# Kernel optimization log

Hardware: AMD Instinct MI355X
Metric: run time of the kernel (lower is better)

## Reference

```python
import jax, jax.numpy as jnp
import numpy as np
from jax import lax

B, T, K, HID, NCLS = 32, 2048, 17, 64, 10
DILATIONS = (1, 1, 2)
RESIDUAL = (False, True, True)
TK = 3  # temporal kernel
BN_EPS = 1e-5
LN_EPS = 1e-5

COCO_EDGES = [(0,1),(0,2),(1,3),(2,4),(5,6),(5,7),(7,9),(6,8),(8,10),(5,11),(6,12),(11,13),(13,15),(12,14),(14,16)]

def build_skeleton_adj(num_kpts=K):
    adj = np.eye(num_kpts, dtype=np.float32)
    for i, j in COCO_EDGES:
        adj[i, j] = 1.0
        adj[j, i] = 1.0
    adj = adj + np.eye(num_kpts, dtype=np.float32)
    deg = adj.sum(axis=1, keepdims=True)
    deg[deg == 0] = 1.0
    return adj / deg

def setup_inputs() -> dict:
    key = jax.random.key(0)
    ks = jax.random.split(key, 8)
    kpts = jax.random.normal(ks[0], (B, T, K, 3), dtype=jnp.float32)
    adj = jnp.asarray(build_skeleton_adj(K))
    gcn_w0 = jax.random.normal(ks[1], (3, HID), dtype=jnp.float32) * (1.0 / np.sqrt(3))
    gcn_w1 = jax.random.normal(ks[2], (HID, HID), dtype=jnp.float32) * (1.0 / np.sqrt(HID))
    gcn_w2 = jax.random.normal(ks[3], (HID, HID), dtype=jnp.float32) * (1.0 / np.sqrt(HID))
    tcn_w = jax.random.normal(ks[4], (3, HID, HID, TK, 1), dtype=jnp.float32) * (1.0 / np.sqrt(HID * TK))
    bn_scale = 1.0 + 0.1 * jax.random.normal(ks[5], (3, HID), dtype=jnp.float32)
    bn_bias = 0.1 * jax.random.normal(ks[6], (3, HID), dtype=jnp.float32)
    bn_mean = 0.1 * jax.random.normal(ks[7], (3, HID), dtype=jnp.float32)
    bn_var = 0.5 + jax.random.uniform(jax.random.fold_in(key, 7), (3, HID), dtype=jnp.float32)
    ln_scale = jnp.ones((HID,), dtype=jnp.float32)
    ln_bias = jnp.zeros((HID,), dtype=jnp.float32)
    fc_w = jax.random.normal(jax.random.fold_in(key, 8), (HID, NCLS), dtype=jnp.float32) * (1.0 / np.sqrt(HID))
    fc_b = jnp.zeros((NCLS,), dtype=jnp.float32)
    return dict(kpts=kpts, adj=adj, gcn_w0=gcn_w0, gcn_w1=gcn_w1, gcn_w2=gcn_w2,
                tcn_w=tcn_w, bn_scale=bn_scale, bn_bias=bn_bias, bn_mean=bn_mean,
                bn_var=bn_var, ln_scale=ln_scale, ln_bias=ln_bias, fc_w=fc_w, fc_b=fc_b)

def _stgn_block(x, adj, gw, tw, bs, bb, bm, bv, dilation, residual):
    # x: [B, C_in, T, K]
    y = jnp.einsum('bctk,kv->bctv', x, adj)          # graph conv over keypoints
    y = jnp.einsum('bitk,io->botk', y, gw)           # channel mixing (intended GCN weight)
    pad = (TK - 1) * dilation // 2
    y = lax.conv_general_dilated(y, tw, window_strides=(1, 1),
                                 padding=[(pad, pad), (0, 0)],
                                 rhs_dilation=(dilation, 1),
                                 dimension_numbers=('NCHW', 'OIHW', 'NCHW'))
    inv = (bs / jnp.sqrt(bv + BN_EPS))[None, :, None, None]
    y = y * inv + (bb - bs * bm / jnp.sqrt(bv + BN_EPS))[None, :, None, None]
    y = jax.nn.relu(y)
    if residual:
        y = y + x
    return y

def reference(kpts, adj, gcn_w0, gcn_w1, gcn_w2, tcn_w, bn_scale, bn_bias, bn_mean,
              bn_var, ln_scale, ln_bias, fc_w, fc_b):
    x = jnp.transpose(kpts, (0, 3, 1, 2))  # [B, 3, T, K]
    gws = (gcn_w0, gcn_w1, gcn_w2)
    for i in range(3):
        x = _stgn_block(x, adj, gws[i], tcn_w[i], bn_scale[i], bn_bias[i],
                        bn_mean[i], bn_var[i], DILATIONS[i], RESIDUAL[i])
    feat = x.mean(axis=(2, 3))  # [B, HID] temporal/spatial mean pool
    mu = feat.mean(axis=-1, keepdims=True)
    var = feat.var(axis=-1, keepdims=True)
    feat = (feat - mu) / jnp.sqrt(var + LN_EPS) * ln_scale + ln_bias
    return feat @ fc_w + fc_b  # [B, NCLS]
```

## Files before the change

kernel.cpp:

```cpp
#include <hip/hip_runtime.h>
#include <hip/hip_fp16.h>
#include <math.h>

#define T_DIM 2048
#define TP_DIM 2052
#define K_DIM 17
#define HID   64
#define B_DIM 32

typedef short s16x8 __attribute__((ext_vector_type(8)));
typedef unsigned u32x2 __attribute__((ext_vector_type(2)));
typedef float f32x4 __attribute__((ext_vector_type(4)));
typedef _Float16 f16x2 __attribute__((ext_vector_type(2)));

__device__ __forceinline__ unsigned pkh(float lo, float hi) {
    return __builtin_bit_cast(unsigned, __builtin_amdgcn_cvt_pkrtz(lo, hi));
}
__device__ __forceinline__ f16x2 u2h(unsigned v) {
    return __builtin_bit_cast(f16x2, v);
}
__device__ __forceinline__ unsigned h2u(f16x2 v) {
    return __builtin_bit_cast(unsigned, v);
}
__device__ __forceinline__ short f2h(float f) {
    _Float16 h = (_Float16)f;
    return __builtin_bit_cast(short, h);
}

static constexpr int NBR_PTR[18] = {0,3,6,9,11,13,17,21,24,27,29,31,34,37,40,43,45,47};
static constexpr int NBR_K[47] = {
    0,1,2,  0,1,3,  0,2,4,  1,3,  2,4,
    5,6,7,11,  5,6,8,12,  5,7,9,  6,8,10,  7,9,  8,10,
    5,11,13,  6,12,14,  11,13,15,  12,14,16,  13,15,  14,16 };
__device__ const int d_NBR_PTR[18] = {0,3,6,9,11,13,17,21,24,27,29,31,34,37,40,43,45,47};
__device__ const int d_NBR_K[47] = {
    0,1,2,  0,1,3,  0,2,4,  1,3,  2,4,
    5,6,7,11,  5,6,8,12,  5,7,9,  6,8,10,  7,9,  8,10,
    5,11,13,  6,12,14,  11,13,15,  12,14,16,  13,15,  14,16 };

__global__ void fold_weights_kernel(
    const float* __restrict__ gw0, const float* __restrict__ gw1,
    const float* __restrict__ gw2, const float* __restrict__ tcn,
    const float* __restrict__ bns, const float* __restrict__ bnb,
    const float* __restrict__ bnm, const float* __restrict__ bnv,
    short* __restrict__ effT0, short* __restrict__ effT12,
    float* __restrict__ bnc)
{
    int tid = blockIdx.x * blockDim.x + threadIdx.x;
    int stride = gridDim.x * blockDim.x;
    for (int idx = tid; idx < 2048; idx += stride) {
        int o = idx >> 5, k = idx & 31, dt = k >> 3, cin = k & 7;
        float s = 0.f;
        if (dt < 3 && cin < 3)
            for (int m = 0; m < 64; m++)
                s += gw0[cin * 64 + m] * tcn[(o * 64 + m) * 3 + dt];
        effT0[idx] = f2h(s);
    }
    for (int idx = tid; idx < 24576; idx += stride) {
        int blk = idx / 12288;
        int r = idx - blk * 12288;
        int o = r / 192, k = r - o * 192, dt = k >> 6, c = k & 63;
        const float* gw = blk ? gw2 : gw1;
        const float* tw = tcn + (size_t)(blk + 1) * 64 * 64 * 3;
        float s = 0.f;
        for (int m = 0; m < 64; m++)
            s += gw[c * 64 + m] * tw[(o * 64 + m) * 3 + dt];
        effT12[idx] = f2h(s);
    }
    for (int i = tid; i < 192; i += stride) {
        float inv = bns[i] * rsqrtf(bnv[i] + 1e-5f);
        bnc[i] = inv;
        bnc[192 + i] = bnb[i] - bnm[i] * inv;
    }
}

__global__ __launch_bounds__(256) void premix_kernel(
    const float* __restrict__ x, const float* __restrict__ adj,
    float* __restrict__ xg, short* __restrict__ y2g, int cb)
{
    const int idx = blockIdx.x * 256 + threadIdx.x;
    const int total = cb * TP_DIM * K_DIM;
    if (idx < total) {
        const int b = idx / (TP_DIM * K_DIM);
        const int rem = idx - b * (TP_DIM * K_DIM);
        const int tp = rem / K_DIM, j = rem - tp * K_DIM;
        const int t = tp - 2;
        float a0 = 0.f, a1 = 0.f, a2 = 0.f;
        if (t >= 0 && t < T_DIM) {
            const float* xp = x + ((size_t)b * T_DIM + t) * 51;
            const int p0 = d_NBR_PTR[j], p1 = d_NBR_PTR[j + 1];
            for (int e = p0; e < p1; e++) {
                int k = d_NBR_K[e];
                float w = adj[k * 17 + j];
                a0 += w * xp[k * 3 + 0];
                a1 += w * xp[k * 3 + 1];
                a2 += w * xp[k * 3 + 2];
            }
        }
        float* op = xg + ((size_t)b * TP_DIM + tp) * 52 + j * 3;
        op[0] = a0; op[1] = a1; op[2] = a2;
    }
    const int zn = cb * 4 * 1088;
    for (int z = idx; z < zn; z += gridDim.x * 256) {
        int bb = z / (4 * 1088);
        int rr = z - bb * 4 * 1088;
        int pi = rr / 1088;
        int ci = rr - pi * 1088;
        int tp = (pi < 2) ? pi : (2048 + pi);
        y2g[((size_t)(bb * TP_DIM + tp) * K_DIM) * 64 + ci] = 0;
    }
}

__global__ __launch_bounds__(256, 4) void stgcn_ab_kernel(
    const float* __restrict__ xg, const float* __restrict__ adj,
    const short* __restrict__ effT0, const short* __restrict__ effT12,
    const float* __restrict__ bnc, short* __restrict__ y2g,
    float* __restrict__ part2, int b0)
{
    __shared__ unsigned adj_h[289];
    __shared__ __align__(16) float xtg[12 * 52];
    __shared__ __align__(16) short ybuf[170 * 72];

    float* pr = (float*)&ybuf[136 * 72];

    const int tid = threadIdx.x;
    const int b = blockIdx.y;
    const int t0 = blockIdx.x * 8;
    const int lane = tid & 63, wave = tid >> 6;
    const int col = lane & 15, kgrp = lane >> 4;

    for (int i = tid; i < 289; i += 256) {
        float w = adj[i];
        adj_h[i] = pkh(w, w);
    }
    {
        const float4* src = (const float4*)(xg + ((size_t)b * TP_DIM + t0) * 52);
        float4* dst = (float4*)xtg;
        for (int i = tid; i < 156; i += 256) dst[i] = src[i];
    }
    s16x8 af1 = *(const s16x8*)(effT0 + (wave * 16 + col) * 32 + kgrp * 8);
    s16x8 af2[6];
    #pragma unroll
    for (int kk = 0; kk < 6; kk++)
        af2[kk] = *(const s16x8*)(effT12 +
            (wave * 16 + col) * 192 + kk * 32 + kgrp * 8);
    __syncthreads();

    {
        f32x4 inv4 = *(const f32x4*)&bnc[wave * 16 + kgrp * 4];
        f32x4 sh4  = *(const f32x4*)&bnc[192 + wave * 16 + kgrp * 4];
        for (int tile = 0; tile < 11; tile++) {
            const int r = tile * 16 + col;
            const int me = r < 170 ? r : 169;
            const int s = (me * 241) >> 12;
            const int j = me - s * 17;
            int4 bz = {0, 0, 0, 0};
            if (kgrp < 3) {
                const float* xp = &xtg[(s + kgrp) * 52 + j * 3];
                bz.x = (int)pkh(xp[0], xp[1]);
                bz.y = (int)pkh(xp[2], 0.f);
            }
            s16x8 bfr = __builtin_bit_cast(s16x8, bz);
            f32x4 acc = __builtin_amdgcn_mfma_f32_16x16x32_f16(
                af1, bfr, (f32x4){0.f, 0.f, 0.f, 0.f}, 0, 0, 0);
            const int t = t0 - 1 + s;
            const bool valid = (t >= 0) && (t < T_DIM);
            if (r < 170) {
                float v0 = valid ? fmaxf(acc[0] * inv4[0] + sh4[0], 0.f) : 0.f;
                float v1 = valid ? fmaxf(acc[1] * inv4[1] + sh4[1], 0.f) : 0.f;
                float v2 = valid ? fmaxf(acc[2] * inv4[2] + sh4[2], 0.f) : 0.f;
                float v3 = valid ? fmaxf(acc[3] * inv4[3] + sh4[3], 0.f) : 0.f;
                u32x2 st; st[0] = pkh(v0, v1); st[1] = pkh(v2, v3);
                *(u32x2*)&ybuf[r * 72 + wave * 16 + kgrp * 4] = st;
            }
        }
    }
    __syncthreads();

    f32x4 acc2[9];
    #pragma unroll
    for (int t2 = 0; t2 < 9; t2++) acc2[t2] = (f32x4){0.f, 0.f, 0.f, 0.f};
    #pragma unroll
    for (int kk = 0; kk < 6; kk++) {
        #pragma unroll
        for (int t2 = 0; t2 < 9; t2++) {
            const int r = t2 * 16 + col;
            const int me = r < 136 ? r : 135;
            s16x8 bfr = *(const s16x8*)&ybuf[
                (me + 17 * (kk >> 1)) * 72 + (kk & 1) * 32 + kgrp * 8];
            acc2[t2] = __builtin_amdgcn_mfma_f32_16x16x32_f16(
                af2[kk], bfr, acc2[t2], 0, 0, 0);
        }
    }
    unsigned rv[17];
    {
        const int tl = tid >> 5, o0 = (tid & 31) * 2;
        #pragma unroll
        for (int v = 0; v < 17; v++)
            rv[v] = *(const unsigned*)&ybuf[((tl + 1) * 17 + v) * 72 + o0];
    }
    __syncthreads();

    #pragma unroll
    for (int t2 = 0; t2 < 9; t2++) {
        const int r = t2 * 16 + col;
        if (r < 136) {
            u32x2 st;
            st[0] = pkh(acc2[t2][0], acc2[t2][1]);
            st[1] = pkh(acc2[t2][2], acc2[t2][3]);
            *(u32x2*)&ybuf[r * 72 + wave * 16 + kgrp * 4] = st;
        }
    }
    __syncthreads();

    {
        const int tl = tid >> 5, o0 = (tid & 31) * 2;
        const f16x2 inv2 = u2h(pkh(bnc[64 + o0], bnc[64 + o0 + 1]));
        const f16x2 sh2  = u2h(pkh(bnc[256 + o0], bnc[256 + o0 + 1]));
        const f16x2 zero = u2h(0u);
        f16x2 zk[17];
        #pragma unroll
        for (int k = 0; k < 17; k++)
            zk[k] = u2h(*(const unsigned*)&ybuf[(tl * 17 + k) * 72 + o0]);
        f16x2 y2v[17];
        f16x2 pool = zero;
        #pragma unroll
        for (int v = 0; v < 17; v++) {
            f16x2 g = zero;
            #pragma unroll
            for (int e = NBR_PTR[v]; e < NBR_PTR[v + 1]; e++) {
                int k = NBR_K[e];
                g = u2h(adj_h[k * 17 + v]) * zk[k] + g;
            }
            f16x2 val = __builtin_elementwise_max(g * inv2 + sh2, zero);
            val = val + u2h(rv[v]);
            y2v[v] = val;
            pool = pool + val;
        }
        const size_t gout = ((size_t)b * TP_DIM + t0 + tl + 2) * K_DIM * 64;
        #pragma unroll
        for (int j = 0; j < 17; j++) {
            f16x2 gg = zero;
            #pragma unroll
            for (int e = NBR_PTR[j]; e < NBR_PTR[j + 1]; e++) {
                int k = NBR_K[e];
                gg = u2h(adj_h[k * 17 + j]) * y2v[k] + gg;
            }
            *(unsigned*)&y2g[gout + (size_t)j * 64 + o0] = h2u(gg);
        }
        pr[tl * 64 + o0]     = (float)pool[0];
        pr[tl * 64 + o0 + 1] = (float)pool[1];
    }
    __syncthreads();
    if (tid < 64) {
        float s = 0.f;
        #pragma unroll
        for (int i = 0; i < 8; i++) s += pr[i * 64 + tid];
        part2[((size_t)(b0 + b) * 256 + blockIdx.x) * 64 + tid] = s;
    }
}

__global__ __launch_bounds__(256, 5) void stgcn_c_kernel(
    const short* __restrict__ y2g, const short* __restrict__ effW3,
    const float* __restrict__ bnc, float* __restrict__ part, int b0)
{
    __shared__ __align__(16) short ybuf[204 * 72];
    __shared__ float pr[64];

    const int tid = threadIdx.x;
    const int b = blockIdx.y;
    const int t0 = blockIdx.x * 8;
    const int lane = tid & 63, wave = tid >> 6;
    const int col = lane & 15, kgrp = lane >> 4;

    s16x8 af3[6];
    #pragma unroll
    for (int kk = 0; kk < 6; kk++)
        af3[kk] = *(const s16x8*)(effW3 +
            (wave * 16 + col) * 192 + kk * 32 + kgrp * 8);
    const f32x4 inv4 = *(const f32x4*)&bnc[128 + wave * 16 + kgrp * 4];
    const f32x4 sh4  = *(const f32x4*)&bnc[320 + wave * 16 + kgrp * 4];

    {
        const short* base = y2g + ((size_t)b * TP_DIM + t0) * K_DIM * 64;
        for (int idx = tid; idx < 1632; idx += 256) {
            const int row = idx >> 3, c = idx & 7;
            *(s16x8*)&ybuf[row * 72 + c * 8] =
                *(const s16x8*)(base + (size_t)row * 64 + c * 8);
        }
    }
    __syncthreads();

    float psum[4] = {0.f, 0.f, 0.f, 0.f};
    for (int t3 = 0; t3 < 9; t3++) {
        const int r = t3 * 16 + col;
        const int me = r < 136 ? r : 135;
        f32x4 acc = (f32x4){0.f, 0.f, 0.f, 0.f};
        #pragma unroll
        for (int kk = 0; kk < 6; kk++) {
            s16x8 bfr = *(const s16x8*)&ybuf[
                (me + 34 * (kk >> 1)) * 72 + (kk & 1) * 32 + kgrp * 8];
            acc = __builtin_amdgcn_mfma_f32_16x16x32_f16(af3[kk], bfr, acc, 0, 0, 0);
        }
        if (r < 136) {
            psum[0] += fmaxf(acc[0] * inv4[0] + sh4[0], 0.f);
            psum[1] += fmaxf(acc[1] * inv4[1] + sh4[1], 0.f);
            psum[2] += fmaxf(acc[2] * inv4[2] + sh4[2], 0.f);
            psum[3] += fmaxf(acc[3] * inv4[3] + sh4[3], 0.f);
        }
    }
    #pragma unroll
    for (int off = 1; off <= 8; off <<= 1) {
        psum[0] += __shfl_xor(psum[0], off);
        psum[1] += __shfl_xor(psum[1], off);
        psum[2] += __shfl_xor(psum[2], off);
        psum[3] += __shfl_xor(psum[3], off);
    }
    if (col == 0)
        *(f32x4*)&pr[wave * 16 + kgrp * 4] =
            (f32x4){psum[0], psum[1], psum[2], psum[3]};
    __syncthreads();
    if (tid < 64)
        part[((size_t)(b0 + b) * 256 + blockIdx.x) * 64 + tid] = pr[tid];
}

__global__ __launch_bounds__(256) void finish_kernel(
    const float* __restrict__ part, const float* __restrict__ part2,
    const float* __restrict__ ln_s, const float* __restrict__ ln_b,
    const float* __restrict__ fc_w, const float* __restrict__ fc_b,
    float* __restrict__ out)
{
    __shared__ float red[4][64];
    __shared__ float ns[64];
    const int b = blockIdx.x;
    const int g = threadIdx.x >> 6, c = threadIdx.x & 63;
    float s = 0.f;
    for (int j = 0; j < 64; j++) {
        size_t i = ((size_t)b * 256 + g * 64 + j) * 64 + c;
        s += part[i] + part2[i];
    }
    red[g][c] = s;
    __syncthreads();
    if (threadIdx.x < 64) {
        float feat = (red[0][c] + red[1][c] + red[2][c] + red[3][c])
                   / (float)(T_DIM * K_DIM);
        float m = feat;
        #pragma unroll
        for (int off = 32; off > 0; off >>= 1) m += __shfl_down(m, off);
        m = __shfl(m, 0) / 64.f;
        float d = feat - m;
        float v = d * d;
        #pragma unroll
        for (int off = 32; off > 0; off >>= 1) v += __shfl_down(v, off);
        v = __shfl(v, 0) / 64.f;
        ns[c] = d * rsqrtf(v + 1e-5f) * ln_s[c] + ln_b[c];
    }
    __syncthreads();
    if (threadIdx.x < 10) {
        float o = fc_b[threadIdx.x];
        for (int i = 0; i < 64; i++) o += ns[i] * fc_w[i * 10 + threadIdx.x];
        out[b * 10 + threadIdx.x] = o;
    }
}

extern "C" void kernel_launch(void* const* d_in, const int* in_sizes, int n_in,
                              void* d_out, int out_size, void* d_ws, size_t ws_size,
                              hipStream_t stream)
{
    const float* kpts = (const float*)d_in[0];
    const float* adj  = (const float*)d_in[1];
    const float* gw0  = (const float*)d_in[2];
    const float* gw1  = (const float*)d_in[3];
    const float* gw2  = (const float*)d_in[4];
    const float* tcn  = (const float*)d_in[5];
    const float* bns  = (const float*)d_in[6];
    const float* bnb  = (const float*)d_in[7];
    const float* bnm  = (const float*)d_in[8];
    const float* bnv  = (const float*)d_in[9];
    const float* lns  = (const float*)d_in[10];
    const float* lnb  = (const float*)d_in[11];
    const float* fcw  = (const float*)d_in[12];
    const float* fcb  = (const float*)d_in[13];
    float* out = (float*)d_out;

    float* bnc   = (float*)d_ws;
    float* part  = bnc + 384;
    float* part2 = part + (size_t)B_DIM * 256 * 64;
    short* effT0  = (short*)(part2 + (size_t)B_DIM * 256 * 64);
    short* effT12 = effT0 + 2048;
    float* xg     = (float*)(effT12 + 24576);
    const size_t fixed_bytes = 384 * 4 + 2 * (size_t)B_DIM * 256 * 64 * 4
                             + 2048 * 2 + 24576 * 2;
    const size_t xg_per_b  = (size_t)TP_DIM * 52 * 4;
    const size_t y2g_per_b = (size_t)TP_DIM * K_DIM * 64 * 2;

    int cb = B_DIM;
    while (cb > 1 &&
           fixed_bytes + (size_t)cb * (xg_per_b + y2g_per_b) > ws_size)
        cb >>= 1;
    short* y2g = (short*)(xg + (size_t)cb * TP_DIM * 52);

    fold_weights_kernel<<<64, 256, 0, stream>>>(gw0, gw1, gw2, tcn,
                                                bns, bnb, bnm, bnv,
                                                effT0, effT12, bnc);

    const int pm_blocks = (cb * TP_DIM * K_DIM + 255) / 256;
    for (int b0 = 0; b0 < B_DIM; b0 += cb) {
        premix_kernel<<<pm_blocks, 256, 0, stream>>>(
            kpts + (size_t)b0 * T_DIM * K_DIM * 3, adj, xg, y2g, cb);
        stgcn_ab_kernel<<<dim3(T_DIM / 8, cb), 256, 0, stream>>>(
            xg, adj, effT0, effT12, bnc, y2g, part2, b0);
        stgcn_c_kernel<<<dim3(T_DIM / 8, cb), 256, 0, stream>>>(
            y2g, effT12 + 12288, bnc, part, b0);
    }

    finish_kernel<<<B_DIM, 256, 0, stream>>>(part, part2, lns, lnb,
                                             fcw, fcb, out);
}
```

Measured before the change: 230.0 us.

## Fuse block-C into AB kernel with halo recompute, dropping global y2g intermediate

The two STGCN kernels are merged into one. Each 8-timestep tile now recomputes a wider halo (14 input timesteps, 12 intermediate timesteps) so the third block's temporal convolution can read its input from LDS instead of a global fp16 y2g buffer. This removes the y2g write and readback, the halo-zeroing pass, one kernel launch and the part2 array. In exchange it adds redundant MFMA and graph-conv work for the halo rows, more LDS per block and extra barriers, which may reduce occupancy.

Result: slower. 235.7 us (+2.5%).

```diff
diff --git a/kernel.cpp b/kernel.cpp
--- a/kernel.cpp
+++ b/kernel.cpp
@@ -3,7 +3,7 @@
 #include <math.h>
 
 #define T_DIM 2048
-#define TP_DIM 2052
+#define TP_DIM 2056
 #define K_DIM 17
 #define HID   64
 #define B_DIM 32
@@ -76,52 +76,42 @@
 
 __global__ __launch_bounds__(256) void premix_kernel(
     const float* __restrict__ x, const float* __restrict__ adj,
-    float* __restrict__ xg, short* __restrict__ y2g, int cb)
+    float* __restrict__ xg, int cb)
 {
     const int idx = blockIdx.x * 256 + threadIdx.x;
     const int total = cb * TP_DIM * K_DIM;
-    if (idx < total) {
-        const int b = idx / (TP_DIM * K_DIM);
-        const int rem = idx - b * (TP_DIM * K_DIM);
-        const int tp = rem / K_DIM, j = rem - tp * K_DIM;
-        const int t = tp - 2;
-        float a0 = 0.f, a1 = 0.f, a2 = 0.f;
-        if (t >= 0 && t < T_DIM) {
-            const float* xp = x + ((size_t)b * T_DIM + t) * 51;
-            const int p0 = d_NBR_PTR[j], p1 = d_NBR_PTR[j + 1];
-            for (int e = p0; e < p1; e++) {
-                int k = d_NBR_K[e];
-                float w = adj[k * 17 + j];
-                a0 += w * xp[k * 3 + 0];
-                a1 += w * xp[k * 3 + 1];
-                a2 += w * xp[k * 3 + 2];
-            }
-        }
-        float* op = xg + ((size_t)b * TP_DIM + tp) * 52 + j * 3;
-        op[0] = a0; op[1] = a1; op[2] = a2;
-    }
-    const int zn = cb * 4 * 1088;
-    for (int z = idx; z < zn; z += gridDim.x * 256) {
-        int bb = z / (4 * 1088);
-        int rr = z - bb * 4 * 1088;
-        int pi = rr / 1088;
-        int ci = rr - pi * 1088;
-        int tp = (pi < 2) ? pi : (2048 + pi);
-        y2g[((size_t)(bb * TP_DIM + tp) * K_DIM) * 64 + ci] = 0;
-    }
-}
-
-__global__ __launch_bounds__(256, 4) void stgcn_ab_kernel(
+    if (idx >= total) return;
+    const int b = idx / (TP_DIM * K_DIM);
+    const int rem = idx - b * (TP_DIM * K_DIM);
+    const int tp = rem / K_DIM, j = rem - tp * K_DIM;
+    const int t = tp - 4;
+    float a0 = 0.f, a1 = 0.f, a2 = 0.f;
+    if (t >= 0 && t < T_DIM) {
+        const float* xp = x + ((size_t)b * T_DIM + t) * 51;
+        const int p0 = d_NBR_PTR[j], p1 = d_NBR_PTR[j + 1];
+        for (int e = p0; e < p1; e++) {
+            int k = d_NBR_K[e];
+            float w = adj[k * 17 + j];
+            a0 += w * xp[k * 3 + 0];
+            a1 += w * xp[k * 3 + 1];
+            a2 += w * xp[k * 3 + 2];
+        }
+    }
+    float* op = xg + ((size_t)b * TP_DIM + tp) * 52 + j * 3;
+    op[0] = a0; op[1] = a1; op[2] = a2;
+}
+
+__global__ __launch_bounds__(256, 4) void stgcn_mono_kernel(
     const float* __restrict__ xg, const float* __restrict__ adj,
     const short* __restrict__ effT0, const short* __restrict__ effT12,
-    const float* __restrict__ bnc, short* __restrict__ y2g,
-    float* __restrict__ part2, int b0)
+    const float* __restrict__ bnc, float* __restrict__ part, int b0)
 {
     __shared__ unsigned adj_h[289];
-    __shared__ __align__(16) float xtg[12 * 52];
-    __shared__ __align__(16) short ybuf[170 * 72];
-
-    float* pr = (float*)&ybuf[136 * 72];
+    __shared__ __align__(16) float xtg[16 * 52];
+    __shared__ __align__(16) short ybuf[238 * 72];
+
+    float* prm = (float*)xtg;
+    float* pr1 = (float*)xtg + 512;
 
     const int tid = threadIdx.x;
     const int b = blockIdx.y;
@@ -136,7 +126,7 @@
     {
         const float4* src = (const float4*)(xg + ((size_t)b * TP_DIM + t0) * 52);
         float4* dst = (float4*)xtg;
-        for (int i = tid; i < 156; i += 256) dst[i] = src[i];
+        for (int i = tid; i < 208; i += 256) dst[i] = src[i];
     }
     s16x8 af1 = *(const s16x8*)(effT0 + (wave * 16 + col) * 32 + kgrp * 8);
     s16x8 af2[6];
@@ -149,9 +139,9 @@
     {
         f32x4 inv4 = *(const f32x4*)&bnc[wave * 16 + kgrp * 4];
         f32x4 sh4  = *(const f32x4*)&bnc[192 + wave * 16 + kgrp * 4];
-        for (int tile = 0; tile < 11; tile++) {
+        for (int tile = 0; tile < 15; tile++) {
             const int r = tile * 16 + col;
-            const int me = r < 170 ? r : 169;
+            const int me = r < 238 ? r : 237;
             const int s = (me * 241) >> 12;
             const int j = me - s * 17;
             int4 bz = {0, 0, 0, 0};
@@ -163,9 +153,9 @@
             s16x8 bfr = __builtin_bit_cast(s16x8, bz);
             f32x4 acc = __builtin_amdgcn_mfma_f32_16x16x32_f16(
                 af1, bfr, (f32x4){0.f, 0.f, 0.f, 0.f}, 0, 0, 0);
-            const int t = t0 - 1 + s;
+            const int t = t0 - 3 + s;
             const bool valid = (t >= 0) && (t < T_DIM);
-            if (r < 170) {
+            if (r < 238) {
                 float v0 = valid ? fmaxf(acc[0] * inv4[0] + sh4[0], 0.f) : 0.f;
                 float v1 = valid ? fmaxf(acc[1] * inv4[1] + sh4[1], 0.f) : 0.f;
                 float v2 = valid ? fmaxf(acc[2] * inv4[2] + sh4[2], 0.f) : 0.f;
@@ -177,168 +167,177 @@
     }
     __syncthreads();
 
-    f32x4 acc2[9];
-    #pragma unroll
-    for (int t2 = 0; t2 < 9; t2++) acc2[t2] = (f32x4){0.f, 0.f, 0.f, 0.f};
+    const int tl0 = tid >> 5, oq = tid & 31, o0 = oq * 2;
+    unsigned rv[2][17];
+    #pragma unroll
+    for (int v = 0; v < 17; v++)
+        rv[0][v] = *(const unsigned*)&ybuf[((tl0 + 1) * 17 + v) * 72 + o0];
+    if (tid < 128) {
+        #pragma unroll
+        for (int v = 0; v < 17; v++)
+            rv[1][v] = *(const unsigned*)&ybuf[((tl0 + 9) * 17 + v) * 72 + o0];
+    }
+
+    f32x4 accA[7];
+    #pragma unroll
+    for (int t2 = 0; t2 < 7; t2++) accA[t2] = (f32x4){0.f, 0.f, 0.f, 0.f};
     #pragma unroll
     for (int kk = 0; kk < 6; kk++) {
         #pragma unroll
-        for (int t2 = 0; t2 < 9; t2++) {
+        for (int t2 = 0; t2 < 7; t2++) {
             const int r = t2 * 16 + col;
-            const int me = r < 136 ? r : 135;
+            s16x8 bfr = *(const s16x8*)&ybuf[
+                (r + 17 * (kk >> 1)) * 72 + (kk & 1) * 32 + kgrp * 8];
+            accA[t2] = __builtin_amdgcn_mfma_f32_16x16x32_f16(
+                af2[kk], bfr, accA[t2], 0, 0, 0);
+        }
+    }
+    __syncthreads();
+
+    #pragma unroll
+    for (int t2 = 0; t2 < 7; t2++) {
+        const int r = t2 * 16 + col;
+        u32x2 st;
+        st[0] = pkh(accA[t2][0], accA[t2][1]);
+        st[1] = pkh(accA[t2][2], accA[t2][3]);
+        *(u32x2*)&ybuf[r * 72 + wave * 16 + kgrp * 4] = st;
+    }
+    f32x4 accB[6];
+    #pragma unroll
+    for (int t2 = 0; t2 < 6; t2++) accB[t2] = (f32x4){0.f, 0.f, 0.f, 0.f};
+    #pragma unroll
+    for (int kk = 0; kk < 6; kk++) {
+        #pragma unroll
+        for (int t2 = 0; t2 < 6; t2++) {
+            const int r = (t2 + 7) * 16 + col;
+            const int me = r < 204 ? r : 203;
             s16x8 bfr = *(const s16x8*)&ybuf[
                 (me + 17 * (kk >> 1)) * 72 + (kk & 1) * 32 + kgrp * 8];
-            acc2[t2] = __builtin_amdgcn_mfma_f32_16x16x32_f16(
-                af2[kk], bfr, acc2[t2], 0, 0, 0);
-        }
-    }
-    unsigned rv[17];
+            accB[t2] = __builtin_amdgcn_mfma_f32_16x16x32_f16(
+                af2[kk], bfr, accB[t2], 0, 0, 0);
+        }
+    }
+    __syncthreads();
+
+    #pragma unroll
+    for (int t2 = 0; t2 < 6; t2++) {
+        const int r = (t2 + 7) * 16 + col;
+        if (r < 204) {
+            u32x2 st;
+            st[0] = pkh(accB[t2][0], accB[t2][1]);
+            st[1] = pkh(accB[t2][2], accB[t2][3]);
+            *(u32x2*)&ybuf[r * 72 + wave * 16 + kgrp * 4] = st;
+        }
+    }
+    __syncthreads();
+
     {
-        const int tl = tid >> 5, o0 = (tid & 31) * 2;
-        #pragma unroll
-        for (int v = 0; v < 17; v++)
-            rv[v] = *(const unsigned*)&ybuf[((tl + 1) * 17 + v) * 72 + o0];
-    }
-    __syncthreads();
-
-    #pragma unroll
-    for (int t2 = 0; t2 < 9; t2++) {
-        const int r = t2 * 16 + col;
-        if (r < 136) {
-            u32x2 st;
-            st[0] = pkh(acc2[t2][0], acc2[t2][1]);
-            st[1] = pkh(acc2[t2][2], acc2[t2][3]);
-            *(u32x2*)&ybuf[r * 72 + wave * 16 + kgrp * 4] = st;
-        }
-    }
-    __syncthreads();
-
-    {
-        const int tl = tid >> 5, o0 = (tid & 31) * 2;
         const f16x2 inv2 = u2h(pkh(bnc[64 + o0], bnc[64 + o0 + 1]));
         const f16x2 sh2  = u2h(pkh(bnc[256 + o0], bnc[256 + o0 + 1]));
         const f16x2 zero = u2h(0u);
-        f16x2 zk[17];
-        #pragma unroll
-        for (int k = 0; k < 17; k++)
-            zk[k] = u2h(*(const unsigned*)&ybuf[(tl * 17 + k) * 72 + o0]);
-        f16x2 y2v[17];
-        f16x2 pool = zero;
-        #pragma unroll
-        for (int v = 0; v < 17; v++) {
-            f16x2 g = zero;
+        #pragma unroll
+        for (int it = 0; it < 2; it++) {
+            const int tl = tl0 + it * 8;
+            if (it == 1 && tid >= 128) break;
+            const int t = t0 - 2 + tl;
+            const bool valid = (t >= 0) && (t < T_DIM);
+            f16x2 zk[17];
             #pragma unroll
-            for (int e = NBR_PTR[v]; e < NBR_PTR[v + 1]; e++) {
-                int k = NBR_K[e];
-                g = u2h(adj_h[k * 17 + v]) * zk[k] + g;
-            }
-            f16x2 val = __builtin_elementwise_max(g * inv2 + sh2, zero);
-            val = val + u2h(rv[v]);
-            y2v[v] = val;
-            pool = pool + val;
-        }
-        const size_t gout = ((size_t)b * TP_DIM + t0 + tl + 2) * K_DIM * 64;
-        #pragma unroll
-        for (int j = 0; j < 17; j++) {
-            f16x2 gg = zero;
+            for (int k = 0; k < 17; k++)
+                zk[k] = u2h(*(const unsigned*)&ybuf[(tl * 17 + k) * 72 + o0]);
+            f16x2 y2v[17];
+            f16x2 pool = zero;
             #pragma unroll
-            for (int e = NBR_PTR[j]; e < NBR_PTR[j + 1]; e++) {
-                int k = NBR_K[e];
-                gg = u2h(adj_h[k * 17 + j]) * y2v[k] + gg;
-            }
-            *(unsigned*)&y2g[gout + (size_t)j * 64 + o0] = h2u(gg);
-        }
-        pr[tl * 64 + o0]     = (float)pool[0];
-        pr[tl * 64 + o0 + 1] = (float)pool[1];
+            for (int v = 0; v < 17; v++) {
+                f16x2 g = zero;
+                #pragma unroll
+                for (int e = NBR_PTR[v]; e < NBR_PTR[v + 1]; e++) {
+                    int k = NBR_K[e];
+                    g = u2h(adj_h[k * 17 + v]) * zk[k] + g;
+                }
+                f16x2 val = __builtin_elementwise_max(g * inv2 + sh2, zero);
+                val = val + u2h(rv[it][v]);
+                if (!valid) val = zero;
+                y2v[v] = val;
+                pool = pool + val;
+            }
+            if (tl >= 2 && tl <= 9) {
+                prm[(tl - 2) * 64 + o0]     = (float)pool[0];
+                prm[(tl - 2) * 64 + o0 + 1] = (float)pool[1];
+            }
+            #pragma unroll
+            for (int j = 0; j < 17; j++) {
+                f16x2 gg = zero;
+                #pragma unroll
+                for (int e = NBR_PTR[j]; e < NBR_PTR[j + 1]; e++) {
+                    int k = NBR_K[e];
+                    gg = u2h(adj_h[k * 17 + j]) * y2v[k] + gg;
+                }
+                *(unsigned*)&ybuf[(tl * 17 + j) * 72 + o0] = h2u(gg);
+            }
+        }
+    }
+    __syncthreads();
+
+    {
+        s16x8 af3[6];
+        #pragma unroll
+        for (int kk = 0; kk < 6; kk++)
+            af3[kk] = *(const s16x8*)(effT12 + 12288 +
+                (wave * 16 + col) * 192 + kk * 32 + kgrp * 8);
+        const f32x4 inv4 = *(const f32x4*)&bnc[128 + wave * 16 + kgrp * 4];
+        const f32x4 sh4  = *(const f32x4*)&bnc[320 + wave * 16 + kgrp * 4];
+        float psum[4] = {0.f, 0.f, 0.f, 0.f};
+        for (int t3 = 0; t3 < 9; t3++) {
+            const int r = t3 * 16 + col;
+            const int me = r < 136 ? r : 135;
+            f32x4 acc = (f32x4){0.f, 0.f, 0.f, 0.f};
+            #pragma unroll
+            for (int kk = 0; kk < 6; kk++) {
+                s16x8 bfr = *(const s16x8*)&ybuf[
+                    (me + 34 * (kk >> 1)) * 72 + (kk & 1) * 32 + kgrp * 8];
+                acc = __builtin_amdgcn_mfma_f32_16x16x32_f16(
+                    af3[kk], bfr, acc, 0, 0, 0);
+            }
+            if (r < 136) {
+                psum[0] += fmaxf(acc[0] * inv4[0] + sh4[0], 0.f);
+                psum[1] += fmaxf(acc[1] * inv4[1] + sh4[1], 0.f);
+                psum[2] += fmaxf(acc[2] * inv4[2] + sh4[2], 0.f);
+                psum[3] += fmaxf(acc[3] * inv4[3] + sh4[3], 0.f);
+            }
+        }
+        #pragma unroll
+        for (int off = 1; off <= 8; off <<= 1) {
+            psum[0] += __shfl_xor(psum[0], off);
+            psum[1] += __shfl_xor(psum[1], off);
+            psum[2] += __shfl_xor(psum[2], off);
+            psum[3] += __shfl_xor(psum[3], off);
+        }
+        if (col == 0)
+            *(f32x4*)&pr1[wave * 16 + kgrp * 4] =
+                (f32x4){psum[0], psum[1], psum[2], psum[3]};
     }
     __syncthreads();
     if (tid < 64) {
-        float s = 0.f;
-        #pragma unroll
-        for (int i = 0; i < 8; i++) s += pr[i * 64 + tid];
-        part2[((size_t)(b0 + b) * 256 + blockIdx.x) * 64 + tid] = s;
-    }
-}
-
-__global__ __launch_bounds__(256, 5) void stgcn_c_kernel(
-    const short* __restrict__ y2g, const short* __restrict__ effW3,
-    const float* __restrict__ bnc, float* __restrict__ part, int b0)
-{
-    __shared__ __align__(16) short ybuf[204 * 72];
-    __shared__ float pr[64];
-
-    const int tid = threadIdx.x;
-    const int b = blockIdx.y;
-    const int t0 = blockIdx.x * 8;
-    const int lane = tid & 63, wave = tid >> 6;
-    const int col = lane & 15, kgrp = lane >> 4;
-
-    s16x8 af3[6];
-    #pragma unroll
-    for (int kk = 0; kk < 6; kk++)
-        af3[kk] = *(const s16x8*)(effW3 +
-            (wave * 16 + col) * 192 + kk * 32 + kgrp * 8);
-    const f32x4 inv4 = *(const f32x4*)&bnc[128 + wave * 16 + kgrp * 4];
-    const f32x4 sh4  = *(const f32x4*)&bnc[320 + wave * 16 + kgrp * 4];
-
-    {
-        const short* base = y2g + ((size_t)b * TP_DIM + t0) * K_DIM * 64;
-        for (int idx = tid; idx < 1632; idx += 256) {
-            const int row = idx >> 3, c = idx & 7;
-            *(s16x8*)&ybuf[row * 72 + c * 8] =
-                *(const s16x8*)(base + (size_t)row * 64 + c * 8);
-        }
-    }
-    __syncthreads();
-
-    float psum[4] = {0.f, 0.f, 0.f, 0.f};
-    for (int t3 = 0; t3 < 9; t3++) {
-        const int r = t3 * 16 + col;
-        const int me = r < 136 ? r : 135;
-        f32x4 acc = (f32x4){0.f, 0.f, 0.f, 0.f};
-        #pragma unroll
-        for (int kk = 0; kk < 6; kk++) {
-            s16x8 bfr = *(const s16x8*)&ybuf[
-                (me + 34 * (kk >> 1)) * 72 + (kk & 1) * 32 + kgrp * 8];
-            acc = __builtin_amdgcn_mfma_f32_16x16x32_f16(af3[kk], bfr, acc, 0, 0, 0);
-        }
-        if (r < 136) {
-            psum[0] += fmaxf(acc[0] * inv4[0] + sh4[0], 0.f);
-            psum[1] += fmaxf(acc[1] * inv4[1] + sh4[1], 0.f);
-            psum[2] += fmaxf(acc[2] * inv4[2] + sh4[2], 0.f);
-            psum[3] += fmaxf(acc[3] * inv4[3] + sh4[3], 0.f);
-        }
-    }
-    #pragma unroll
-    for (int off = 1; off <= 8; off <<= 1) {
-        psum[0] += __shfl_xor(psum[0], off);
-        psum[1] += __shfl_xor(psum[1], off);
-        psum[2] += __shfl_xor(psum[2], off);
-        psum[3] += __shfl_xor(psum[3], off);
-    }
-    if (col == 0)
-        *(f32x4*)&pr[wave * 16 + kgrp * 4] =
-            (f32x4){psum[0], psum[1], psum[2], psum[3]};
-    __syncthreads();
-    if (tid < 64)
-        part[((size_t)(b0 + b) * 256 + blockIdx.x) * 64 + tid] = pr[tid];
+        float s = pr1[tid];
+        #pragma unroll
+        for (int i = 0; i < 8; i++) s += prm[i * 64 + tid];
+        part[((size_t)(b0 + b) * 256 + blockIdx.x) * 64 + tid] = s;
+    }
 }
 
 __global__ __launch_bounds__(256) void finish_kernel(
-    const float* __restrict__ part, const float* __restrict__ part2,
-    const float* __restrict__ ln_s, const float* __restrict__ ln_b,
-    const float* __restrict__ fc_w, const float* __restrict__ fc_b,
-    float* __restrict__ out)
+    const float* __restrict__ part, const float* __restrict__ ln_s,
+    const float* __restrict__ ln_b, const float* __restrict__ fc_w,
+    const float* __restrict__ fc_b, float* __restrict__ out)
 {
     __shared__ float red[4][64];
     __shared__ float ns[64];
     const int b = blockIdx.x;
     const int g = threadIdx.x >> 6, c = threadIdx.x & 63;
     float s = 0.f;
-    for (int j = 0; j < 64; j++) {
-        size_t i = ((size_t)b * 256 + g * 64 + j) * 64 + c;
-        s += part[i] + part2[i];
-    }
+    for (int j = 0; j < 64; j++)
+        s += part[((size_t)b * 256 + g * 64 + j) * 64 + c];
     red[g][c] = s;
     __syncthreads();
     if (threadIdx.x < 64) {
@@ -383,22 +382,17 @@
     const float* fcb  = (const float*)d_in[13];
     float* out = (float*)d_out;
 
-    float* bnc   = (float*)d_ws;
-    float* part  = bnc + 384;
-    float* part2 = part + (size_t)B_DIM * 256 * 64;
-    short* effT0  = (short*)(part2 + (size_t)B_DIM * 256 * 64);
+    float* bnc  = (float*)d_ws;
+    float* part = bnc + 384;
+    short* effT0  = (short*)(part + (size_t)B_DIM * 256 * 64);
     short* effT12 = effT0 + 2048;
-    float* xg     = (float*)(effT12 + 24576);
-    const size_t fixed_bytes = 384 * 4 + 2 * (size_t)B_DIM * 256 * 64 * 4
+    float* xg = (float*)(effT12 + 24576);
+    const size_t fixed_bytes = 384 * 4 + (size_t)B_DIM * 256 * 64 * 4
                              + 2048 * 2 + 24576 * 2;
-    const size_t xg_per_b  = (size_t)TP_DIM * 52 * 4;
-    const size_t y2g_per_b = (size_t)TP_DIM * K_DIM * 64 * 2;
+    const size_t xg_per_b = (size_t)TP_DIM * 52 * 4;
 
     int cb = B_DIM;
-    while (cb > 1 &&
-           fixed_bytes + (size_t)cb * (xg_per_b + y2g_per_b) > ws_size)
-        cb >>= 1;
-    short* y2g = (short*)(xg + (size_t)cb * TP_DIM * 52);
+    while (cb > 1 && fixed_bytes + (size_t)cb * xg_per_b > ws_size) cb >>= 1;
 
     fold_weights_kernel<<<64, 256, 0, stream>>>(gw0, gw1, gw2, tcn,
                                                 bns, bnb, bnm, bnv,
@@ -407,13 +401,10 @@
     const int pm_blocks = (cb * TP_DIM * K_DIM + 255) / 256;
     for (int b0 = 0; b0 < B_DIM; b0 += cb) {
         premix_kernel<<<pm_blocks, 256, 0, stream>>>(
-            kpts + (size_t)b0 * T_DIM * K_DIM * 3, adj, xg, y2g, cb);
-        stgcn_ab_kernel<<<dim3(T_DIM / 8, cb), 256, 0, stream>>>(
-            xg, adj, effT0, effT12, bnc, y2g, part2, b0);
-        stgcn_c_kernel<<<dim3(T_DIM / 8, cb), 256, 0, stream>>>(
-            y2g, effT12 + 12288, bnc, part, b0);
-    }
-
-    finish_kernel<<<B_DIM, 256, 0, stream>>>(part, part2, lns, lnb,
-                                             fcw, fcb, out);
-}
+            kpts + (size_t)b0 * T_DIM * K_DIM * 3, adj, xg, cb);
+        stgcn_mono_kernel<<<dim3(T_DIM / 8, cb), 256, 0, stream>>>(
+            xg, adj, effT0, effT12, bnc, part, b0);
+    }
+
+    finish_kernel<<<B_DIM, 256, 0, stream>>>(part, lns, lnb, fcw, fcb, out);
+}
```
